# Optimization experiments

Measured on AMD Instinct MI355X. Metric: run time of the kernel, lower is better.

The kernel has to match this reference:

```python
import jax, jax.numpy as jnp
import numpy as np


def setup_inputs() -> dict:
    key = jax.random.key(0)
    k1, k2, k3 = jax.random.split(key, 3)
    B, M, N, D = 8, 12, 32, 256
    C = N * N          # Conv2d channel dim == N*N (see permute/view in source)
    R = 2              # reduction
    x = jax.random.normal(k1, (B, M, N, D), dtype=jnp.float32)
    W1 = jax.random.normal(k2, (C // R, C), dtype=jnp.float32) * 0.02  # Conv2d(C, C//R, 1, bias=False)
    W2 = jax.random.normal(k3, (C, C // R), dtype=jnp.float32) * 0.02  # Conv2d(C//R, C, 1, bias=False)
    return {"x": x, "W1": W1, "W2": W2}


def _mycorr(x):
    # Pearson correlation across feature dim D -> [B, M, N, N] adjacency
    xm = x - x.mean(axis=-1, keepdims=True)
    cov = jnp.einsum('bmnd,bmkd->bmnk', xm, xm)
    diag = jnp.diagonal(cov, axis1=-2, axis2=-1)                 # [B, M, N]
    norm = jnp.sqrt(jnp.clip(diag, 1e-12))
    return cov / (norm[..., :, None] * norm[..., None, :])


def reference(x, W1, W2):
    B, M, N, D = x.shape
    adj = _mycorr(x)

    # Fused pairwise-combo + mean over concat dim (2D):
    #   cat([Wh_i, pos_ij * Wh_j], -1).mean(-1) = (sum_d Wh_i + sum_d pos_ij*Wh_j) / (2D)
    # pos_ij[d] = 1 where Wh_i[d] == Wh_j[d] else 2   (source's where(diff==0, 1, 2))
    Wi = x[:, :, :, None, :]          # [B, M, N, 1, D]
    Wj = x[:, :, None, :, :]          # [B, M, 1, N, D]
    pos = jnp.where(Wi == Wj, jnp.float32(1.0), jnp.float32(2.0))
    e0 = (x.sum(-1)[:, :, :, None] + (pos * Wj).sum(-1)) / (2.0 * D)  # [B, M, N, N]

    # squeeze-excite style 1x1-conv MLP over the N*N channel dim
    ef = e0.reshape(B, M, N * N).transpose(0, 2, 1)                   # [B, C=N*N, M]
    h = jax.nn.relu(jnp.einsum('oc,bcm->bom', W1, ef))                # [B, C//R, M]
    e2 = jnp.einsum('co,bom->bcm', W2, h)                             # [B, C, M]
    e = jax.nn.sigmoid(e2.transpose(0, 2, 1).reshape(B, M, N, N))

    att = jnp.where(adj > 0, e, jnp.float32(-1e12))
    att = jax.nn.softmax(att, axis=-1)
    return jnp.einsum('bmnk,bmkd->bmnd', att, x)
```

## Files before the change

### kernel.cpp

```cpp
#include <hip/hip_runtime.h>


__device__ __forceinline__ float dot4(float4 a, float4 b) {
    return a.x*b.x + a.y*b.y + a.z*b.z + a.w*b.w;
}
__device__ __forceinline__ void fma4(float4& acc, float s, float4 v) {
    acc.x += s*v.x; acc.y += s*v.y; acc.z += s*v.z; acc.w += s*v.w;
}

__global__ __launch_bounds__(512) void kA(const float* __restrict__ x,
                                          const float* __restrict__ W1,
                                          float* __restrict__ W1A,
                                          float* __restrict__ Ssum) {
    __shared__ float w[16][1024];
    const int t = threadIdx.x, bid = blockIdx.x;
    if (bid < 32) {
        const float4* W14 = (const float4*)(W1 + bid*16384);
        float4* w4 = (float4*)&w[0][0];
        #pragma unroll
        for (int i = 0; i < 8; ++i) w4[t + 512*i] = W14[t + 512*i];
        __syncthreads();
        const int ol = t >> 5, n = t & 31;
        const float* row = &w[ol][0];
        float T1 = 0.f, T2 = 0.f;
        #pragma unroll
        for (int k = 0; k < 32; ++k) T1 += row[n*32 + ((k + n) & 31)];
        #pragma unroll
        for (int m = 0; m < 32; ++m) T2 += row[m*32 + n];
        float diag = row[n*33];
        W1A[(bid*16 + ol)*32 + n] = (T1 + 2.f*T2 - diag) * (1.f/512.f);
    } else {
        const int g = bid - 32;
        const float4* x4 = (const float4*)x;
        const int n = t >> 4, dq = t & 15;
        #pragma unroll
        for (int bl = 0; bl < 8; ++bl) {
            const float4* xb = x4 + (g*8 + bl)*2048;
            float s = 0.f;
            #pragma unroll
            for (int j = 0; j < 4; ++j) {
                float4 v = xb[n*64 + dq + 16*j];
                s += v.x + v.y + v.z + v.w;
            }
            s += __shfl_xor(s, 1, 16);
            s += __shfl_xor(s, 2, 16);
            s += __shfl_xor(s, 4, 16);
            s += __shfl_xor(s, 8, 16);
            if (dq == 0) Ssum[(g*8 + bl)*32 + n] = s;
        }
    }
}

__global__ __launch_bounds__(512) void kB(const float* __restrict__ W1A,
                                          const float* __restrict__ Ssum,
                                          const float* __restrict__ W2,
                                          float* __restrict__ Et) {
    __shared__ float S_l[8][32];
    __shared__ float hl[8][512];
    const int t = threadIdx.x;
    const int cQ = blockIdx.x, g = blockIdx.y;
    if (t < 256) ((float*)S_l)[t] = Ssum[g*256 + t];
    __syncthreads();
    {
        const float4* wa = (const float4*)(W1A + t*32);
        float4 w0=wa[0], w1=wa[1], w2=wa[2], w3=wa[3],
               w4=wa[4], w5=wa[5], w6=wa[6], w7=wa[7];
        #pragma unroll
        for (int bl = 0; bl < 8; ++bl) {
            const float4* s4 = (const float4*)&S_l[bl][0];
            float a = dot4(w0,s4[0]) + dot4(w1,s4[1]) + dot4(w2,s4[2]) +
                      dot4(w3,s4[3]) + dot4(w4,s4[4]) + dot4(w5,s4[5]) +
                      dot4(w6,s4[6]) + dot4(w7,s4[7]);
            hl[bl][t] = fmaxf(a, 0.f);
        }
    }
    __syncthreads();
    const int olane = t & 31, cgp = t >> 5;
    const int c0 = cQ*64 + cgp;
    const float4* w4a = (const float4*)(W2 + (c0     )*512);
    const float4* w4b = (const float4*)(W2 + (c0 + 16)*512);
    const float4* w4c = (const float4*)(W2 + (c0 + 32)*512);
    const float4* w4d = (const float4*)(W2 + (c0 + 48)*512);
    float accA[8] = {0.f,0.f,0.f,0.f,0.f,0.f,0.f,0.f};
    float accB[8] = {0.f,0.f,0.f,0.f,0.f,0.f,0.f,0.f};
    float accC[8] = {0.f,0.f,0.f,0.f,0.f,0.f,0.f,0.f};
    float accD[8] = {0.f,0.f,0.f,0.f,0.f,0.f,0.f,0.f};
    #pragma unroll
    for (int oo = 0; oo < 4; ++oo) {
        float4 hv[8];
        #pragma unroll
        for (int bl = 0; bl < 8; ++bl)
            hv[bl] = *((const float4*)&hl[bl][(oo*32 + olane)*4]);
        float4 wa = w4a[oo*32 + olane];
        float4 wb = w4b[oo*32 + olane];
        float4 wc = w4c[oo*32 + olane];
        float4 wd = w4d[oo*32 + olane];
        #pragma unroll
        for (int bl = 0; bl < 8; ++bl) {
            accA[bl] += dot4(wa, hv[bl]);
            accB[bl] += dot4(wb, hv[bl]);
            accC[bl] += dot4(wc, hv[bl]);
            accD[bl] += dot4(wd, hv[bl]);
        }
    }
    #pragma unroll
    for (int bl = 0; bl < 8; ++bl) {
        float a = accA[bl], b = accB[bl], c = accC[bl], d = accD[bl];
        #pragma unroll
        for (int m = 1; m < 32; m <<= 1) {
            a += __shfl_xor(a, m, 32);
            b += __shfl_xor(b, m, 32);
            c += __shfl_xor(c, m, 32);
            d += __shfl_xor(d, m, 32);
        }
        accA[bl]=a; accB[bl]=b; accC[bl]=c; accD[bl]=d;
    }
    if (olane == 0) {
        #pragma unroll
        for (int bl = 0; bl < 8; ++bl) {
            int row = (g*8 + bl)*1024;
            Et[row + c0]      = 1.f/(1.f + __expf(-accA[bl]));
            Et[row + c0 + 16] = 1.f/(1.f + __expf(-accB[bl]));
            Et[row + c0 + 32] = 1.f/(1.f + __expf(-accC[bl]));
            Et[row + c0 + 48] = 1.f/(1.f + __expf(-accD[bl]));
        }
    }
}

__global__ __launch_bounds__(512) void kC(const float* __restrict__ x,
                                          const float* __restrict__ Et,
                                          float* __restrict__ out) {
    __shared__ float4 xs4[32][65];
    __shared__ float att[32][36];
    __shared__ float S_l[32];
    const int t = threadIdx.x;
    const int bm = blockIdx.x >> 1, hh = blockIdx.x & 1;
    const float4* x4 = (const float4*)x;

    #pragma unroll
    for (int i = 0; i < 4; ++i) {
        int idx = t + 512*i;
        xs4[idx >> 6][idx & 63] = x4[bm*2048 + idx];
    }
    __syncthreads();
    {
        int r = t >> 4, dq = t & 15;
        float s = 0.f;
        #pragma unroll
        for (int j = 0; j < 4; ++j) {
            float4 v = xs4[r][dq + 16*j];
            s += v.x + v.y + v.z + v.w;
        }
        s += __shfl_xor(s, 1, 16);
        s += __shfl_xor(s, 2, 16);
        s += __shfl_xor(s, 4, 16);
        s += __shfl_xor(s, 8, 16);
        if (dq == 0) S_l[r] = s;
    }
    __syncthreads();
    if (t < 256) {
        int a = t >> 4, b = t & 15;
        float g00=0.f, g01=0.f, g10=0.f, g11=0.f;
        #pragma unroll 8
        for (int q = 0; q < 64; ++q) {
            float4 a0 = xs4[a][q],    a1 = xs4[a+16][q];
            float4 b0 = xs4[b][q],    b1 = xs4[b+16][q];
            g00 += dot4(a0,b0); g01 += dot4(a0,b1);
            g10 += dot4(a1,b0); g11 += dot4(a1,b1);
        }
        float sa0 = S_l[a]    * (1.f/256.f);
        float sa1 = S_l[a+16] * (1.f/256.f);
        float sb0 = S_l[b], sb1 = S_l[b+16];
        const float* Eb = Et + bm*1024;
        float e00 = Eb[a*32 + b];
        float e01 = Eb[a*32 + b+16];
        float e10 = Eb[(a+16)*32 + b];
        float e11 = Eb[(a+16)*32 + b+16];
        att[a][b]       = (g00 - sa0*sb0) > 0.f ? e00 : -1e12f;
        att[a][b+16]    = (g01 - sa0*sb1) > 0.f ? e01 : -1e12f;
        att[a+16][b]    = (g10 - sa1*sb0) > 0.f ? e10 : -1e12f;
        att[a+16][b+16] = (g11 - sa1*sb1) > 0.f ? e11 : -1e12f;
    }
    __syncthreads();
    {
        int r = t >> 4, q = t & 15;
        float2 lg = *((const float2*)&att[r][q*2]);
        float m = fmaxf(lg.x, lg.y);
        m = fmaxf(m, __shfl_xor(m,1,16));
        m = fmaxf(m, __shfl_xor(m,2,16));
        m = fmaxf(m, __shfl_xor(m,4,16));
        m = fmaxf(m, __shfl_xor(m,8,16));
        float2 p;
        p.x = __expf(lg.x-m); p.y = __expf(lg.y-m);
        float s = p.x + p.y;
        s += __shfl_xor(s,1,16);
        s += __shfl_xor(s,2,16);
        s += __shfl_xor(s,4,16);
        s += __shfl_xor(s,8,16);
        float inv = 1.f/s;
        p.x*=inv; p.y*=inv;
        *((float2*)&att[r][q*2]) = p;
    }
    __syncthreads();
    {
        int txl = t & 31, wy = t >> 5;
        int r0 = wy*2;
        float4 acc0={0,0,0,0}, acc1={0,0,0,0};
        #pragma unroll
        for (int kq = 0; kq < 8; ++kq) {
            float4 xa = xs4[kq*4+0][hh*32 + txl];
            float4 xb = xs4[kq*4+1][hh*32 + txl];
            float4 xc = xs4[kq*4+2][hh*32 + txl];
            float4 xd = xs4[kq*4+3][hh*32 + txl];
            float4 w0 = *((const float4*)&att[r0+0][kq*4]);
            float4 w1 = *((const float4*)&att[r0+1][kq*4]);
            fma4(acc0,w0.x,xa); fma4(acc0,w0.y,xb); fma4(acc0,w0.z,xc); fma4(acc0,w0.w,xd);
            fma4(acc1,w1.x,xa); fma4(acc1,w1.y,xb); fma4(acc1,w1.z,xc); fma4(acc1,w1.w,xd);
        }
        float4* out4 = (float4*)out;
        int base = bm*2048 + hh*32 + txl;
        out4[base + (r0+0)*64] = acc0;
        out4[base + (r0+1)*64] = acc1;
    }
}

extern "C" void kernel_launch(void* const* d_in, const int* in_sizes, int n_in,
                              void* d_out, int out_size, void* d_ws, size_t ws_size,
                              hipStream_t stream) {
    const float* x  = (const float*)d_in[0];
    const float* W1 = (const float*)d_in[1];
    const float* W2 = (const float*)d_in[2];
    float* out = (float*)d_out;
    float* ws  = (float*)d_ws;

    float* W1A  = ws;
    float* Ssum = ws + 16384;
    float* Et   = ws + 19456;

    kA<<<44, 512, 0, stream>>>(x, W1, W1A, Ssum);
    kB<<<dim3(16, 12), 512, 0, stream>>>(W1A, Ssum, W2, Et);
    kC<<<192, 512, 0, stream>>>(x, Et, out);
}
```

Measured before the change: 88.53 us.

## Fuse three kernels into one with per-group atomic grid barriers

Merges the three launches (W1 reduction plus row sums, the squeeze-excite MLP, and the correlation/softmax/aggregation) into a single 192-block kernel. Blocks are split into 12 groups of 16 that synchronise through device-scope atomic counters with spin-waits. The first barrier guards the W1A and Ssum results, the second guards Et. Each group recomputes the full W1A reduction redundantly so it never waits on other groups, which removes the launch gaps between stages. The cost is 12x more W1 reads, spin-wait overhead, and reliance on relaxed atomics and every block of a group being resident at once.

```diff
diff --git a/kernel.cpp b/kernel.cpp
--- a/kernel.cpp
+++ b/kernel.cpp
@@ -1,5 +1,11 @@
 #include <hip/hip_runtime.h>
 
+
+#define NGRP 12
+
+__device__ unsigned int g_bar0[NGRP * 32];
+__device__ unsigned int g_bar1[NGRP * 32];
+__device__ unsigned int g_done[NGRP * 32];
 
 __device__ __forceinline__ float dot4(float4 a, float4 b) {
     return a.x*b.x + a.y*b.y + a.z*b.z + a.w*b.w;
@@ -8,133 +14,46 @@
     acc.x += s*v.x; acc.y += s*v.y; acc.z += s*v.z; acc.w += s*v.w;
 }
 
-__global__ __launch_bounds__(512) void kA(const float* __restrict__ x,
-                                          const float* __restrict__ W1,
-                                          float* __restrict__ W1A,
-                                          float* __restrict__ Ssum) {
-    __shared__ float w[16][1024];
-    const int t = threadIdx.x, bid = blockIdx.x;
-    if (bid < 32) {
-        const float4* W14 = (const float4*)(W1 + bid*16384);
-        float4* w4 = (float4*)&w[0][0];
-        #pragma unroll
-        for (int i = 0; i < 8; ++i) w4[t + 512*i] = W14[t + 512*i];
-        __syncthreads();
-        const int ol = t >> 5, n = t & 31;
-        const float* row = &w[ol][0];
-        float T1 = 0.f, T2 = 0.f;
-        #pragma unroll
-        for (int k = 0; k < 32; ++k) T1 += row[n*32 + ((k + n) & 31)];
-        #pragma unroll
-        for (int m = 0; m < 32; ++m) T2 += row[m*32 + n];
-        float diag = row[n*33];
-        W1A[(bid*16 + ol)*32 + n] = (T1 + 2.f*T2 - diag) * (1.f/512.f);
-    } else {
-        const int g = bid - 32;
-        const float4* x4 = (const float4*)x;
-        const int n = t >> 4, dq = t & 15;
-        #pragma unroll
-        for (int bl = 0; bl < 8; ++bl) {
-            const float4* xb = x4 + (g*8 + bl)*2048;
-            float s = 0.f;
-            #pragma unroll
-            for (int j = 0; j < 4; ++j) {
-                float4 v = xb[n*64 + dq + 16*j];
-                s += v.x + v.y + v.z + v.w;
-            }
-            s += __shfl_xor(s, 1, 16);
-            s += __shfl_xor(s, 2, 16);
-            s += __shfl_xor(s, 4, 16);
-            s += __shfl_xor(s, 8, 16);
-            if (dq == 0) Ssum[(g*8 + bl)*32 + n] = s;
-        }
-    }
-}
-
-__global__ __launch_bounds__(512) void kB(const float* __restrict__ W1A,
-                                          const float* __restrict__ Ssum,
-                                          const float* __restrict__ W2,
-                                          float* __restrict__ Et) {
-    __shared__ float S_l[8][32];
-    __shared__ float hl[8][512];
+__device__ __forceinline__ void st_agent(float* p, float v) {
+    __hip_atomic_store(p, v, __ATOMIC_RELAXED, __HIP_MEMORY_SCOPE_AGENT);
+}
+__device__ __forceinline__ float ld_agent(const float* p) {
+    return __hip_atomic_load(p, __ATOMIC_RELAXED, __HIP_MEMORY_SCOPE_AGENT);
+}
+__device__ __forceinline__ unsigned long long ld_agent64(const unsigned long long* p) {
+    return __hip_atomic_load(p, __ATOMIC_RELAXED, __HIP_MEMORY_SCOPE_AGENT);
+}
+
+__device__ __forceinline__ void bar_arrive(unsigned int* ctr) {
+    __syncthreads();
+    if (threadIdx.x == 0)
+        __hip_atomic_fetch_add(ctr, 1u, __ATOMIC_RELAXED, __HIP_MEMORY_SCOPE_AGENT);
+}
+__device__ __forceinline__ void bar_wait(unsigned int* ctr) {
+    if (threadIdx.x == 0) {
+        while (__hip_atomic_load(ctr, __ATOMIC_RELAXED, __HIP_MEMORY_SCOPE_AGENT) < 16u)
+            __builtin_amdgcn_s_sleep(2);
+    }
+    __syncthreads();
+}
+
+__global__ __launch_bounds__(512) void fused(
+        const float* __restrict__ x, const float* __restrict__ W1,
+        const float* __restrict__ W2, float* __restrict__ out,
+        float* __restrict__ W1A, float* __restrict__ Ssum,
+        float* __restrict__ Et)
+{
+    __shared__ float4 xs4[32][65];
+    __shared__ float  w[16][1024];
+    __shared__ float  hl[8][512];
+    __shared__ float  att[32][36];
+    __shared__ float  S_l8[8][32];
+    __shared__ float  S_loc[32];
     const int t = threadIdx.x;
-    const int cQ = blockIdx.x, g = blockIdx.y;
-    if (t < 256) ((float*)S_l)[t] = Ssum[g*256 + t];
-    __syncthreads();
-    {
-        const float4* wa = (const float4*)(W1A + t*32);
-        float4 w0=wa[0], w1=wa[1], w2=wa[2], w3=wa[3],
-               w4=wa[4], w5=wa[5], w6=wa[6], w7=wa[7];
-        #pragma unroll
-        for (int bl = 0; bl < 8; ++bl) {
-            const float4* s4 = (const float4*)&S_l[bl][0];
-            float a = dot4(w0,s4[0]) + dot4(w1,s4[1]) + dot4(w2,s4[2]) +
-                      dot4(w3,s4[3]) + dot4(w4,s4[4]) + dot4(w5,s4[5]) +
-                      dot4(w6,s4[6]) + dot4(w7,s4[7]);
-            hl[bl][t] = fmaxf(a, 0.f);
-        }
-    }
-    __syncthreads();
-    const int olane = t & 31, cgp = t >> 5;
-    const int c0 = cQ*64 + cgp;
-    const float4* w4a = (const float4*)(W2 + (c0     )*512);
-    const float4* w4b = (const float4*)(W2 + (c0 + 16)*512);
-    const float4* w4c = (const float4*)(W2 + (c0 + 32)*512);
-    const float4* w4d = (const float4*)(W2 + (c0 + 48)*512);
-    float accA[8] = {0.f,0.f,0.f,0.f,0.f,0.f,0.f,0.f};
-    float accB[8] = {0.f,0.f,0.f,0.f,0.f,0.f,0.f,0.f};
-    float accC[8] = {0.f,0.f,0.f,0.f,0.f,0.f,0.f,0.f};
-    float accD[8] = {0.f,0.f,0.f,0.f,0.f,0.f,0.f,0.f};
-    #pragma unroll
-    for (int oo = 0; oo < 4; ++oo) {
-        float4 hv[8];
-        #pragma unroll
-        for (int bl = 0; bl < 8; ++bl)
-            hv[bl] = *((const float4*)&hl[bl][(oo*32 + olane)*4]);
-        float4 wa = w4a[oo*32 + olane];
-        float4 wb = w4b[oo*32 + olane];
-        float4 wc = w4c[oo*32 + olane];
-        float4 wd = w4d[oo*32 + olane];
-        #pragma unroll
-        for (int bl = 0; bl < 8; ++bl) {
-            accA[bl] += dot4(wa, hv[bl]);
-            accB[bl] += dot4(wb, hv[bl]);
-            accC[bl] += dot4(wc, hv[bl]);
-            accD[bl] += dot4(wd, hv[bl]);
-        }
-    }
-    #pragma unroll
-    for (int bl = 0; bl < 8; ++bl) {
-        float a = accA[bl], b = accB[bl], c = accC[bl], d = accD[bl];
-        #pragma unroll
-        for (int m = 1; m < 32; m <<= 1) {
-            a += __shfl_xor(a, m, 32);
-            b += __shfl_xor(b, m, 32);
-            c += __shfl_xor(c, m, 32);
-            d += __shfl_xor(d, m, 32);
-        }
-        accA[bl]=a; accB[bl]=b; accC[bl]=c; accD[bl]=d;
-    }
-    if (olane == 0) {
-        #pragma unroll
-        for (int bl = 0; bl < 8; ++bl) {
-            int row = (g*8 + bl)*1024;
-            Et[row + c0]      = 1.f/(1.f + __expf(-accA[bl]));
-            Et[row + c0 + 16] = 1.f/(1.f + __expf(-accB[bl]));
-            Et[row + c0 + 32] = 1.f/(1.f + __expf(-accC[bl]));
-            Et[row + c0 + 48] = 1.f/(1.f + __expf(-accD[bl]));
-        }
-    }
-}
-
-__global__ __launch_bounds__(512) void kC(const float* __restrict__ x,
-                                          const float* __restrict__ Et,
-                                          float* __restrict__ out) {
-    __shared__ float4 xs4[32][65];
-    __shared__ float att[32][36];
-    __shared__ float S_l[32];
-    const int t = threadIdx.x;
-    const int bm = blockIdx.x >> 1, hh = blockIdx.x & 1;
+    const int bid = blockIdx.x;
+    const int g = bid >> 4;
+    const int gi = g * 32;
+    const int bm = bid >> 1, hh = bid & 1;
     const float4* x4 = (const float4*)x;
 
     #pragma unroll
@@ -155,31 +74,140 @@
         s += __shfl_xor(s, 2, 16);
         s += __shfl_xor(s, 4, 16);
         s += __shfl_xor(s, 8, 16);
-        if (dq == 0) S_l[r] = s;
-    }
-    __syncthreads();
+        if (dq == 0) S_loc[r] = s;
+    }
+    __syncthreads();
+    if (hh == 0 && t < 32) st_agent(&Ssum[bm*32 + t], S_loc[t]);
+    {
+        const int oT = bid & 15;
+        #pragma unroll
+        for (int rnd = 0; rnd < 2; ++rnd) {
+            const float4* W14 = (const float4*)(W1 + (oT*32 + rnd*16)*1024);
+            float4* w4 = (float4*)&w[0][0];
+            #pragma unroll
+            for (int i = 0; i < 8; ++i) w4[t + 512*i] = W14[t + 512*i];
+            __syncthreads();
+            const int ol = t >> 5, n = t & 31;
+            const float* row = &w[ol][0];
+            float T1 = 0.f, T2 = 0.f;
+            #pragma unroll
+            for (int k = 0; k < 32; ++k) T1 += row[n*32 + ((k + n) & 31)];
+            #pragma unroll
+            for (int m = 0; m < 32; ++m) T2 += row[m*32 + n];
+            float diag = row[n*33];
+            st_agent(&W1A[(oT*32 + rnd*16 + ol)*32 + n],
+                     (T1 + 2.f*T2 - diag) * (1.f/512.f));
+            __syncthreads();
+        }
+    }
+    bar_arrive(&g_bar0[gi]);
+
+    const int ga = t >> 4, gb = t & 15;
+    float g00=0.f, g01=0.f, g10=0.f, g11=0.f;
+    float sa0=0.f, sa1=0.f, sb0=0.f, sb1=0.f;
     if (t < 256) {
-        int a = t >> 4, b = t & 15;
-        float g00=0.f, g01=0.f, g10=0.f, g11=0.f;
         #pragma unroll 8
         for (int q = 0; q < 64; ++q) {
-            float4 a0 = xs4[a][q],    a1 = xs4[a+16][q];
-            float4 b0 = xs4[b][q],    b1 = xs4[b+16][q];
+            float4 a0 = xs4[ga][q],    a1 = xs4[ga+16][q];
+            float4 b0 = xs4[gb][q],    b1 = xs4[gb+16][q];
             g00 += dot4(a0,b0); g01 += dot4(a0,b1);
             g10 += dot4(a1,b0); g11 += dot4(a1,b1);
         }
-        float sa0 = S_l[a]    * (1.f/256.f);
-        float sa1 = S_l[a+16] * (1.f/256.f);
-        float sb0 = S_l[b], sb1 = S_l[b+16];
+        sa0 = S_loc[ga]    * (1.f/256.f);
+        sa1 = S_loc[ga+16] * (1.f/256.f);
+        sb0 = S_loc[gb];
+        sb1 = S_loc[gb+16];
+    }
+    bar_wait(&g_bar0[gi]);
+
+    {
+        if (t < 256) ((float*)S_l8)[t] = ld_agent(&Ssum[g*256 + t]);
+        __syncthreads();
+        {
+            const unsigned long long* wrow =
+                (const unsigned long long*)(W1A + t*32);
+            float wv[32];
+            #pragma unroll
+            for (int i = 0; i < 16; ++i) {
+                unsigned long long v = ld_agent64(wrow + i);
+                wv[2*i]   = __uint_as_float((unsigned)(v & 0xffffffffu));
+                wv[2*i+1] = __uint_as_float((unsigned)(v >> 32));
+            }
+            #pragma unroll
+            for (int bl = 0; bl < 8; ++bl) {
+                const float* sb = &S_l8[bl][0];
+                float a = 0.f;
+                #pragma unroll
+                for (int n = 0; n < 32; ++n) a += wv[n] * sb[n];
+                hl[bl][t] = fmaxf(a, 0.f);
+            }
+        }
+        __syncthreads();
+        const int cQ = bid & 15;
+        const int olane = t & 31, cgp = t >> 5;
+        const int c0 = cQ*64 + cgp;
+        const float4* w4a = (const float4*)(W2 + (c0     )*512);
+        const float4* w4b = (const float4*)(W2 + (c0 + 16)*512);
+        const float4* w4c = (const float4*)(W2 + (c0 + 32)*512);
+        const float4* w4d = (const float4*)(W2 + (c0 + 48)*512);
+        float accA[8] = {0.f,0.f,0.f,0.f,0.f,0.f,0.f,0.f};
+        float accB[8] = {0.f,0.f,0.f,0.f,0.f,0.f,0.f,0.f};
+        float accC[8] = {0.f,0.f,0.f,0.f,0.f,0.f,0.f,0.f};
+        float accD[8] = {0.f,0.f,0.f,0.f,0.f,0.f,0.f,0.f};
+        #pragma unroll
+        for (int oo = 0; oo < 4; ++oo) {
+            float4 hv[8];
+            #pragma unroll
+            for (int bl = 0; bl < 8; ++bl)
+                hv[bl] = *((const float4*)&hl[bl][(oo*32 + olane)*4]);
+            float4 wa = w4a[oo*32 + olane];
+            float4 wb = w4b[oo*32 + olane];
+            float4 wc = w4c[oo*32 + olane];
+            float4 wd = w4d[oo*32 + olane];
+            #pragma unroll
+            for (int bl = 0; bl < 8; ++bl) {
+                accA[bl] += dot4(wa, hv[bl]);
+                accB[bl] += dot4(wb, hv[bl]);
+                accC[bl] += dot4(wc, hv[bl]);
+                accD[bl] += dot4(wd, hv[bl]);
+            }
+        }
+        #pragma unroll
+        for (int bl = 0; bl < 8; ++bl) {
+            float a = accA[bl], b = accB[bl], c = accC[bl], d = accD[bl];
+            #pragma unroll
+            for (int m = 1; m < 32; m <<= 1) {
+                a += __shfl_xor(a, m, 32);
+                b += __shfl_xor(b, m, 32);
+                c += __shfl_xor(c, m, 32);
+                d += __shfl_xor(d, m, 32);
+            }
+            accA[bl]=a; accB[bl]=b; accC[bl]=c; accD[bl]=d;
+        }
+        if (olane == 0) {
+            #pragma unroll
+            for (int bl = 0; bl < 8; ++bl) {
+                int row = (g*8 + bl)*1024;
+                st_agent(&Et[row + c0],      1.f/(1.f + __expf(-accA[bl])));
+                st_agent(&Et[row + c0 + 16], 1.f/(1.f + __expf(-accB[bl])));
+                st_agent(&Et[row + c0 + 32], 1.f/(1.f + __expf(-accC[bl])));
+                st_agent(&Et[row + c0 + 48], 1.f/(1.f + __expf(-accD[bl])));
+            }
+        }
+    }
+    bar_arrive(&g_bar1[gi]);
+    bar_wait(&g_bar1[gi]);
+
+    if (t < 256) {
         const float* Eb = Et + bm*1024;
-        float e00 = Eb[a*32 + b];
-        float e01 = Eb[a*32 + b+16];
-        float e10 = Eb[(a+16)*32 + b];
-        float e11 = Eb[(a+16)*32 + b+16];
-        att[a][b]       = (g00 - sa0*sb0) > 0.f ? e00 : -1e12f;
-        att[a][b+16]    = (g01 - sa0*sb1) > 0.f ? e01 : -1e12f;
-        att[a+16][b]    = (g10 - sa1*sb0) > 0.f ? e10 : -1e12f;
-        att[a+16][b+16] = (g11 - sa1*sb1) > 0.f ? e11 : -1e12f;
+        float e00 = ld_agent(&Eb[ga*32 + gb]);
+        float e01 = ld_agent(&Eb[ga*32 + gb+16]);
+        float e10 = ld_agent(&Eb[(ga+16)*32 + gb]);
+        float e11 = ld_agent(&Eb[(ga+16)*32 + gb+16]);
+        att[ga][gb]       = (g00 - sa0*sb0) > 0.f ? e00 : -1e12f;
+        att[ga][gb+16]    = (g01 - sa0*sb1) > 0.f ? e01 : -1e12f;
+        att[ga+16][gb]    = (g10 - sa1*sb0) > 0.f ? e10 : -1e12f;
+        att[ga+16][gb+16] = (g11 - sa1*sb1) > 0.f ? e11 : -1e12f;
     }
     __syncthreads();
     {
@@ -222,6 +250,16 @@
         out4[base + (r0+0)*64] = acc0;
         out4[base + (r0+1)*64] = acc1;
     }
+
+    if (t == 0) {
+        unsigned int old = __hip_atomic_fetch_add(&g_done[gi], 1u,
+                              __ATOMIC_RELAXED, __HIP_MEMORY_SCOPE_AGENT);
+        if (old == 15u) {
+            __hip_atomic_store(&g_bar0[gi], 0u, __ATOMIC_RELAXED, __HIP_MEMORY_SCOPE_AGENT);
+            __hip_atomic_store(&g_bar1[gi], 0u, __ATOMIC_RELAXED, __HIP_MEMORY_SCOPE_AGENT);
+            __hip_atomic_store(&g_done[gi], 0u, __ATOMIC_RELAXED, __HIP_MEMORY_SCOPE_AGENT);
+        }
+    }
 }
 
 extern "C" void kernel_launch(void* const* d_in, const int* in_sizes, int n_in,
@@ -237,7 +275,5 @@
     float* Ssum = ws + 16384;
     float* Et   = ws + 19456;
 
-    kA<<<44, 512, 0, stream>>>(x, W1, W1A, Ssum);
-    kB<<<dim3(16, 12), 512, 0, stream>>>(W1A, Ssum, W2, Et);
-    kC<<<192, 512, 0, stream>>>(x, Et, out);
-}
+    fused<<<192, 512, 0, stream>>>(x, W1, W2, out, W1A, Ssum, Et);
+}
```

After: 88.43 us. About the same (-0.1%).
